# Performance work log

Hardware: AMD Instinct MI355X
Metric: run time of the kernel (lower is better)

The kernel has to match this reference:

```python
import jax, jax.numpy as jnp
import numpy as np

RADIUS = 2  # half window; original kernel truncates the spatial Gaussian at ~2.5*sigma


def setup_inputs() -> dict:
    key = jax.random.key(0)
    input_img = jax.random.normal(key, (2, 1, 128, 128, 128), dtype=jnp.float32)
    return {
        "input_img": input_img,
        "sigma_x": jnp.float32(1.0),
        "sigma_y": jnp.float32(1.0),
        "sigma_z": jnp.float32(1.0),
        "color_sigma": jnp.float32(0.5),
    }


def reference(input_img, sigma_x, sigma_y, sigma_z, color_sigma):
    # 3D bilateral filter: out(i) = sum_k w_spatial(k) * w_range(x_i, x_k) * x_k / sum_k w
    R = RADIUS
    pad = [(0, 0), (0, 0), (R, R), (R, R), (R, R)]
    xp = jnp.pad(input_img, pad)                       # zero-padded volume
    mp = jnp.pad(jnp.ones_like(input_img), pad)        # validity mask (out-of-bounds taps excluded)

    offs = np.array([(dx, dy, dz)
                     for dx in range(-R, R + 1)
                     for dy in range(-R, R + 1)
                     for dz in range(-R, R + 1)], dtype=np.int32)  # (K,3), K=125
    d2 = jnp.asarray(offs.astype(np.float32) ** 2)     # squared offsets (K,3)
    w_sp = jnp.exp(-(d2[:, 0] / (2.0 * sigma_x ** 2)
                     + d2[:, 1] / (2.0 * sigma_y ** 2)
                     + d2[:, 2] / (2.0 * sigma_z ** 2)))  # (K,)
    starts = jnp.asarray(offs + R)                     # slice starts into the padded volume

    inv_2cs2 = 1.0 / (2.0 * color_sigma ** 2)
    shape = input_img.shape

    def body(carry, inp):
        num, den = carry
        start, ws = inp
        s = jnp.concatenate([jnp.zeros(2, jnp.int32), start])
        xk = jax.lax.dynamic_slice(xp, s, shape)       # shifted neighbor volume
        mk = jax.lax.dynamic_slice(mp, s, shape)
        w = ws * mk * jnp.exp(-(input_img - xk) ** 2 * inv_2cs2)
        return (num + w * xk, den + w), None

    zero = jnp.zeros_like(input_img)
    (num, den), _ = jax.lax.scan(body, (zero, zero), (starts, w_sp))
    return num / den
```

## Files before the change

### kernel.cpp

```cpp
#include <hip/hip_runtime.h>
#include <hip/hip_bf16.h>


#define RADIUS 2
#define N 128
#define TX 16
#define TY 8
#define TZ 8
#define PITCH (TX + 2 * RADIUS)
#define LYD (TY + 2 * RADIUS)
#define LZD (TZ + 2 * RADIUS)
#define LDS_SIZE (PITCH * LYD * LZD)

#define LOG2E 1.4426950408889634f
#define BIG 1.0e18f
#define EXP2_SCALE 8388608.0f
#define EXP2_BIAS 1065353216.0f

typedef float f32x2 __attribute__((ext_vector_type(2)));

__global__ __launch_bounds__(256, 4) void bilateral3d_kernel(
    const float* __restrict__ in, const float* __restrict__ p_sx,
    const float* __restrict__ p_sy, const float* __restrict__ p_sz,
    const float* __restrict__ p_cs, float* __restrict__ out) {
  __shared__ float s[LDS_SIZE];

  const int tid = threadIdx.x;
  const int x0 = blockIdx.x * TX;
  const int y0 = blockIdx.y * TY;
  const int zb = blockIdx.z;
  const int z0 = (zb & 15) * TZ;
  const int b = zb >> 4;

  const float* vol = in + (size_t)b * (N * N * N);

  for (int i = tid; i < LDS_SIZE; i += 256) {
    int lx = i % PITCH;
    int t = i / PITCH;
    int ly = t % LYD;
    int lz = t / LYD;
    int gx = x0 + lx - RADIUS;
    int gy = y0 + ly - RADIUS;
    int gz = z0 + lz - RADIUS;
    float v = BIG;
    if ((unsigned)gx < N && (unsigned)gy < N && (unsigned)gz < N)
      v = vol[((size_t)gz * N + gy) * N + gx];
    s[i] = v;
  }
  __syncthreads();

  const int tx = tid & 3;
  const int ty = (tid >> 2) & 7;
  const int tz = tid >> 5;

  const float sxv = p_sx[0], syv = p_sy[0], szv = p_sz[0], csv = p_cs[0];
  const float AX2 = EXP2_SCALE * LOG2E / (2.0f * sxv * sxv);
  const float AY2 = EXP2_SCALE * LOG2E / (2.0f * syv * syv);
  const float AZ2 = EXP2_SCALE * LOG2E / (2.0f * szv * szv);
  const float AX2_4 = 4.0f * AX2;
  const float sR = __builtin_sqrtf(EXP2_SCALE * LOG2E / (2.0f * csv * csv));
  f32x2 S2;
  S2.x = sR;
  S2.y = sR;

  const int xw = 4 * tx;

  const int cbase = ((tz + RADIUS) * LYD + (ty + RADIUS)) * PITCH + xw;
  const float xs0 = s[cbase + 2] * sR;
  const float xs1 = s[cbase + 3] * sR;
  const float xs2 = s[cbase + 4] * sR;
  const float xs3 = s[cbase + 5] * sR;
  f32x2 XS0, XS1, XS2, XS3;
  XS0.x = xs0; XS0.y = xs0;
  XS1.x = xs1; XS1.y = xs1;
  XS2.x = xs2; XS2.y = xs2;
  XS3.x = xs3; XS3.y = xs3;

  f32x2 NU0 = {0.f, 0.f}, NU1 = {0.f, 0.f}, NU2 = {0.f, 0.f}, NU3 = {0.f, 0.f};
  f32x2 DE0 = {0.f, 0.f}, DE1 = {0.f, 0.f}, DE2 = {0.f, 0.f}, DE3 = {0.f, 0.f};
  float ns0 = 0, ns1 = 0, ns2 = 0, ns3 = 0;
  float es0 = 0, es1 = 0, es2 = 0, es3 = 0;

#define PK(XS2V, GS, GR, CC2, NUM2, DEN2)                                \
  {                                                                      \
    f32x2 _t, _e;                                                        \
    asm("v_pk_add_f32 %0, %1, %2 neg_lo:[0,1] neg_hi:[0,1]"              \
        : "=v"(_t) : "v"(XS2V), "v"(GS));                                \
    asm("v_pk_fma_f32 %0, %1, %1, %2 neg_lo:[0,1,0] neg_hi:[0,1,0]"      \
        : "=v"(_e) : "v"(_t), "v"(CC2));                                 \
    unsigned _ql, _qh;                                                   \
    asm("v_cvt_u32_f32 %0, %1" : "=v"(_ql) : "v"(_e.x));                 \
    asm("v_cvt_u32_f32 %0, %1" : "=v"(_qh) : "v"(_e.y));                 \
    f32x2 _w;                                                            \
    _w.x = __uint_as_float(_ql);                                         \
    _w.y = __uint_as_float(_qh);                                         \
    asm("v_pk_add_f32 %0, %0, %1" : "+v"(DEN2) : "v"(_w));               \
    asm("v_pk_fma_f32 %0, %1, %2, %0" : "+v"(NUM2) : "v"(_w), "v"(GR));  \
  }

#define SC(XSV, FS, FR, CC, NN, EE)                      \
  {                                                      \
    float _t = (XSV) - (FS);                             \
    float _f = fmaf(_t, -_t, (CC));                      \
    unsigned _q;                                         \
    asm("v_cvt_u32_f32 %0, %1" : "=v"(_q) : "v"(_f));    \
    float _w = __uint_as_float(_q);                      \
    EE += _w;                                            \
    NN = fmaf(_w, (FR), NN);                             \
  }

#pragma unroll 1
  for (int dz = -RADIUS; dz <= RADIUS; ++dz) {
    const float pz2 = AZ2 * (float)(dz * dz);
    const int zrow = (tz + RADIUS + dz) * LYD;
#pragma unroll
    for (int dy = -RADIUS; dy <= RADIUS; ++dy) {
      const float cc0 = EXP2_BIAS - (pz2 + AY2 * (float)(dy * dy));
      const float cm1 = cc0 - AX2;
      const float cm4 = cc0 - AX2_4;
      f32x2 P41, P01, P10, P14;
      P41.x = cm4; P41.y = cm1;
      P01.x = cc0; P01.y = cm1;
      P10.x = cm1; P10.y = cc0;
      P14.x = cm1; P14.y = cm4;

      const int rb = (zrow + (ty + RADIUS + dy)) * PITCH + xw;
      const f32x2 G0 = *(const f32x2*)&s[rb];
      const f32x2 G1 = *(const f32x2*)&s[rb + 2];
      const f32x2 G2 = *(const f32x2*)&s[rb + 4];
      const f32x2 G3 = *(const f32x2*)&s[rb + 6];
      f32x2 Gs0, Gs1, Gs2, Gs3;
      asm("v_pk_mul_f32 %0, %1, %2" : "=v"(Gs0) : "v"(G0), "v"(S2));
      asm("v_pk_mul_f32 %0, %1, %2" : "=v"(Gs1) : "v"(G1), "v"(S2));
      asm("v_pk_mul_f32 %0, %1, %2" : "=v"(Gs2) : "v"(G2), "v"(S2));
      asm("v_pk_mul_f32 %0, %1, %2" : "=v"(Gs3) : "v"(G3), "v"(S2));

      PK(XS0, Gs0, G0, P41, NU0, DE0)
      PK(XS0, Gs1, G1, P01, NU0, DE0)
      SC(xs0, Gs2.x, G2.x, cm4, ns0, es0)
      SC(xs1, Gs0.y, G0.y, cm4, ns1, es1)
      PK(XS1, Gs1, G1, P10, NU1, DE1)
      PK(XS1, Gs2, G2, P14, NU1, DE1)
      PK(XS2, Gs1, G1, P41, NU2, DE2)
      PK(XS2, Gs2, G2, P01, NU2, DE2)
      SC(xs2, Gs3.x, G3.x, cm4, ns2, es2)
      SC(xs3, Gs1.y, G1.y, cm4, ns3, es3)
      PK(XS3, Gs2, G2, P10, NU3, DE3)
      PK(XS3, Gs3, G3, P14, NU3, DE3)
    }
  }

  float4 r;
  r.x = (NU0.x + NU0.y + ns0) / (DE0.x + DE0.y + es0);
  r.y = (NU1.x + NU1.y + ns1) / (DE1.x + DE1.y + es1);
  r.z = (NU2.x + NU2.y + ns2) / (DE2.x + DE2.y + es2);
  r.w = (NU3.x + NU3.y + ns3) / (DE3.x + DE3.y + es3);

  const int gz = z0 + tz, gy = y0 + ty;
  *(float4*)&out[(((size_t)b * N + gz) * N + gy) * N + (x0 + xw)] = r;
}

extern "C" void kernel_launch(void* const* d_in, const int* in_sizes, int n_in,
                              void* d_out, int out_size, void* d_ws, size_t ws_size,
                              hipStream_t stream) {
  const float* in = (const float*)d_in[0];
  const float* sx = (const float*)d_in[1];
  const float* sy = (const float*)d_in[2];
  const float* sz = (const float*)d_in[3];
  const float* cs = (const float*)d_in[4];
  float* out = (float*)d_out;

  dim3 grid(N / TX, N / TY, (N / TZ) * 2);
  bilateral3d_kernel<<<grid, 256, 0, stream>>>(in, sx, sy, sz, cs, out);
}
```

Measured before the change: 137.6 us.

## Use fp16 exponent-trick weights and packed fp16 accumulation in bilateral filter

Pre-scales the LDS tile by the range sigma when loading and stores an extra fp16 copy of it. The exp2 trick now builds fp16 bit patterns: a fmax against a magic constant plus a byte perm packs two weights into one register, replacing the float-to-uint converts. Numerator and denominator are accumulated with packed fp16 add and fma, which cuts VALU work per tap. In exchange, fp16 accumulation over 125 taps loses precision and the weight approximation gets coarser, which may exceed the accuracy tolerance.

```diff
diff --git a/kernel.cpp b/kernel.cpp
--- a/kernel.cpp
+++ b/kernel.cpp
@@ -14,16 +14,27 @@
 
 #define LOG2E 1.4426950408889634f
 #define BIG 1.0e18f
-#define EXP2_SCALE 8388608.0f
-#define EXP2_BIAS 1065353216.0f
+#define MAGIC 8388608.0f
+#define BASE16 8403968.0f
 
 typedef float f32x2 __attribute__((ext_vector_type(2)));
+typedef _Float16 h16x2 __attribute__((ext_vector_type(2)));
+
+static __device__ __forceinline__ float lo_f(unsigned u) {
+  h16x2 t = __builtin_bit_cast(h16x2, u);
+  return (float)t.x;
+}
+static __device__ __forceinline__ float hi_f(unsigned u) {
+  h16x2 t = __builtin_bit_cast(h16x2, u);
+  return (float)t.y;
+}
 
 __global__ __launch_bounds__(256, 4) void bilateral3d_kernel(
     const float* __restrict__ in, const float* __restrict__ p_sx,
     const float* __restrict__ p_sy, const float* __restrict__ p_sz,
     const float* __restrict__ p_cs, float* __restrict__ out) {
   __shared__ float s[LDS_SIZE];
+  __shared__ _Float16 h[LDS_SIZE];
 
   const int tid = threadIdx.x;
   const int x0 = blockIdx.x * TX;
@@ -31,6 +42,14 @@
   const int zb = blockIdx.z;
   const int z0 = (zb & 15) * TZ;
   const int b = zb >> 4;
+
+  const float sxv = p_sx[0], syv = p_sy[0], szv = p_sz[0], csv = p_cs[0];
+  const float K10 = 1024.0f * LOG2E;
+  const float AX2 = K10 / (2.0f * sxv * sxv);
+  const float AY2 = K10 / (2.0f * syv * syv);
+  const float AZ2 = K10 / (2.0f * szv * szv);
+  const float AX2_4 = 4.0f * AX2;
+  const float sR = __builtin_sqrtf(K10 / (2.0f * csv * csv));
 
   const float* vol = in + (size_t)b * (N * N * N);
 
@@ -45,7 +64,9 @@
     float v = BIG;
     if ((unsigned)gx < N && (unsigned)gy < N && (unsigned)gz < N)
       v = vol[((size_t)gz * N + gy) * N + gx];
-    s[i] = v;
+    float vs = v * sR;
+    s[i] = vs;
+    h[i] = (_Float16)__builtin_fminf(vs, 60000.0f);
   }
   __syncthreads();
 
@@ -53,60 +74,50 @@
   const int ty = (tid >> 2) & 7;
   const int tz = tid >> 5;
 
-  const float sxv = p_sx[0], syv = p_sy[0], szv = p_sz[0], csv = p_cs[0];
-  const float AX2 = EXP2_SCALE * LOG2E / (2.0f * sxv * sxv);
-  const float AY2 = EXP2_SCALE * LOG2E / (2.0f * syv * syv);
-  const float AZ2 = EXP2_SCALE * LOG2E / (2.0f * szv * szv);
-  const float AX2_4 = 4.0f * AX2;
-  const float sR = __builtin_sqrtf(EXP2_SCALE * LOG2E / (2.0f * csv * csv));
-  f32x2 S2;
-  S2.x = sR;
-  S2.y = sR;
-
   const int xw = 4 * tx;
 
   const int cbase = ((tz + RADIUS) * LYD + (ty + RADIUS)) * PITCH + xw;
-  const float xs0 = s[cbase + 2] * sR;
-  const float xs1 = s[cbase + 3] * sR;
-  const float xs2 = s[cbase + 4] * sR;
-  const float xs3 = s[cbase + 5] * sR;
+  const float xs0 = s[cbase + 2];
+  const float xs1 = s[cbase + 3];
+  const float xs2 = s[cbase + 4];
+  const float xs3 = s[cbase + 5];
   f32x2 XS0, XS1, XS2, XS3;
   XS0.x = xs0; XS0.y = xs0;
   XS1.x = xs1; XS1.y = xs1;
   XS2.x = xs2; XS2.y = xs2;
   XS3.x = xs3; XS3.y = xs3;
 
-  f32x2 NU0 = {0.f, 0.f}, NU1 = {0.f, 0.f}, NU2 = {0.f, 0.f}, NU3 = {0.f, 0.f};
-  f32x2 DE0 = {0.f, 0.f}, DE1 = {0.f, 0.f}, DE2 = {0.f, 0.f}, DE3 = {0.f, 0.f};
-  float ns0 = 0, ns1 = 0, ns2 = 0, ns3 = 0;
-  float es0 = 0, es1 = 0, es2 = 0, es3 = 0;
-
-#define PK(XS2V, GS, GR, CC2, NUM2, DEN2)                                \
-  {                                                                      \
-    f32x2 _t, _e;                                                        \
-    asm("v_pk_add_f32 %0, %1, %2 neg_lo:[0,1] neg_hi:[0,1]"              \
-        : "=v"(_t) : "v"(XS2V), "v"(GS));                                \
-    asm("v_pk_fma_f32 %0, %1, %1, %2 neg_lo:[0,1,0] neg_hi:[0,1,0]"      \
-        : "=v"(_e) : "v"(_t), "v"(CC2));                                 \
-    unsigned _ql, _qh;                                                   \
-    asm("v_cvt_u32_f32 %0, %1" : "=v"(_ql) : "v"(_e.x));                 \
-    asm("v_cvt_u32_f32 %0, %1" : "=v"(_qh) : "v"(_e.y));                 \
-    f32x2 _w;                                                            \
-    _w.x = __uint_as_float(_ql);                                         \
-    _w.y = __uint_as_float(_qh);                                         \
-    asm("v_pk_add_f32 %0, %0, %1" : "+v"(DEN2) : "v"(_w));               \
-    asm("v_pk_fma_f32 %0, %1, %2, %0" : "+v"(NUM2) : "v"(_w), "v"(GR));  \
-  }
-
-#define SC(XSV, FS, FR, CC, NN, EE)                      \
-  {                                                      \
-    float _t = (XSV) - (FS);                             \
-    float _f = fmaf(_t, -_t, (CC));                      \
-    unsigned _q;                                         \
-    asm("v_cvt_u32_f32 %0, %1" : "=v"(_q) : "v"(_f));    \
-    float _w = __uint_as_float(_q);                      \
-    EE += _w;                                            \
-    NN = fmaf(_w, (FR), NN);                             \
+  const unsigned* hw = (const unsigned*)h;
+
+  unsigned NUa0 = 0, NUa1 = 0, NUa2 = 0, NUa3 = 0;
+  unsigned DEa0 = 0, DEa1 = 0, DEa2 = 0, DEa3 = 0;
+  unsigned NUs01 = 0, NUs23 = 0, DEs01 = 0, DEs23 = 0;
+
+#define PK(XS2V, GS, H16, CC2, NUM, DEN)                                   \
+  {                                                                        \
+    f32x2 _t, _y;                                                          \
+    asm("v_pk_add_f32 %0, %1, %2 neg_lo:[0,1] neg_hi:[0,1]"                \
+        : "=v"(_t) : "v"(XS2V), "v"(GS));                                  \
+    asm("v_pk_fma_f32 %0, %1, %1, %2 neg_lo:[0,1,0] neg_hi:[0,1,0]"        \
+        : "=v"(_y) : "v"(_t), "v"(CC2));                                   \
+    float _ax = __builtin_fmaxf(_y.x, MAGIC);                              \
+    float _ay = __builtin_fmaxf(_y.y, MAGIC);                              \
+    unsigned _w = __builtin_amdgcn_perm(__float_as_uint(_ay),              \
+                                        __float_as_uint(_ax), 0x05040100); \
+    asm("v_pk_add_f16 %0, %0, %1" : "+v"(DEN) : "v"(_w));                  \
+    asm("v_pk_fma_f16 %0, %1, %2, %0" : "+v"(NUM) : "v"(_w), "v"(H16));    \
+  }
+
+#define SC2(XA, XB, GA, GB, H16, CC, NUM, DEN)                             \
+  {                                                                        \
+    float _ta = (XA) - (GA);                                               \
+    float _tb = (XB) - (GB);                                               \
+    float _ya = __builtin_fmaxf(fmaf(_ta, -_ta, (CC)), MAGIC);             \
+    float _yb = __builtin_fmaxf(fmaf(_tb, -_tb, (CC)), MAGIC);             \
+    unsigned _w = __builtin_amdgcn_perm(__float_as_uint(_yb),              \
+                                        __float_as_uint(_ya), 0x05040100); \
+    asm("v_pk_add_f16 %0, %0, %1" : "+v"(DEN) : "v"(_w));                  \
+    asm("v_pk_fma_f16 %0, %1, %2, %0" : "+v"(NUM) : "v"(_w), "v"(H16));    \
   }
 
 #pragma unroll 1
@@ -115,7 +126,7 @@
     const int zrow = (tz + RADIUS + dz) * LYD;
 #pragma unroll
     for (int dy = -RADIUS; dy <= RADIUS; ++dy) {
-      const float cc0 = EXP2_BIAS - (pz2 + AY2 * (float)(dy * dy));
+      const float cc0 = BASE16 - (pz2 + AY2 * (float)(dy * dy));
       const float cm1 = cc0 - AX2;
       const float cm4 = cc0 - AX2_4;
       f32x2 P41, P01, P10, P14;
@@ -129,32 +140,46 @@
       const f32x2 G1 = *(const f32x2*)&s[rb + 2];
       const f32x2 G2 = *(const f32x2*)&s[rb + 4];
       const f32x2 G3 = *(const f32x2*)&s[rb + 6];
-      f32x2 Gs0, Gs1, Gs2, Gs3;
-      asm("v_pk_mul_f32 %0, %1, %2" : "=v"(Gs0) : "v"(G0), "v"(S2));
-      asm("v_pk_mul_f32 %0, %1, %2" : "=v"(Gs1) : "v"(G1), "v"(S2));
-      asm("v_pk_mul_f32 %0, %1, %2" : "=v"(Gs2) : "v"(G2), "v"(S2));
-      asm("v_pk_mul_f32 %0, %1, %2" : "=v"(Gs3) : "v"(G3), "v"(S2));
-
-      PK(XS0, Gs0, G0, P41, NU0, DE0)
-      PK(XS0, Gs1, G1, P01, NU0, DE0)
-      SC(xs0, Gs2.x, G2.x, cm4, ns0, es0)
-      SC(xs1, Gs0.y, G0.y, cm4, ns1, es1)
-      PK(XS1, Gs1, G1, P10, NU1, DE1)
-      PK(XS1, Gs2, G2, P14, NU1, DE1)
-      PK(XS2, Gs1, G1, P41, NU2, DE2)
-      PK(XS2, Gs2, G2, P01, NU2, DE2)
-      SC(xs2, Gs3.x, G3.x, cm4, ns2, es2)
-      SC(xs3, Gs1.y, G1.y, cm4, ns3, es3)
-      PK(XS3, Gs2, G2, P10, NU3, DE3)
-      PK(XS3, Gs3, G3, P14, NU3, DE3)
+      const int hb = rb >> 1;
+      const unsigned H0 = hw[hb];
+      const unsigned H1 = hw[hb + 1];
+      const unsigned H2 = hw[hb + 2];
+      const unsigned H3 = hw[hb + 3];
+
+      PK(XS0, G0, H0, P41, NUa0, DEa0)
+      PK(XS0, G1, H1, P01, NUa0, DEa0)
+      PK(XS1, G1, H1, P10, NUa1, DEa1)
+      PK(XS1, G2, H2, P14, NUa1, DEa1)
+      PK(XS2, G1, H1, P41, NUa2, DEa2)
+      PK(XS2, G2, H2, P01, NUa2, DEa2)
+      PK(XS3, G2, H2, P10, NUa3, DEa3)
+      PK(XS3, G3, H3, P14, NUa3, DEa3)
+
+      {
+        unsigned Ga16 = __builtin_amdgcn_perm(H0, H2, 0x07060100);
+        SC2(xs0, xs1, G2.x, G0.y, Ga16, cm4, NUs01, DEs01)
+      }
+      {
+        unsigned Gb16 = __builtin_amdgcn_perm(H1, H3, 0x07060100);
+        SC2(xs2, xs3, G3.x, G1.y, Gb16, cm4, NUs23, DEs23)
+      }
     }
   }
 
+  const float num0 = lo_f(NUa0) + hi_f(NUa0) + lo_f(NUs01);
+  const float num1 = lo_f(NUa1) + hi_f(NUa1) + hi_f(NUs01);
+  const float num2 = lo_f(NUa2) + hi_f(NUa2) + lo_f(NUs23);
+  const float num3 = lo_f(NUa3) + hi_f(NUa3) + hi_f(NUs23);
+  const float den0 = lo_f(DEa0) + hi_f(DEa0) + lo_f(DEs01);
+  const float den1 = lo_f(DEa1) + hi_f(DEa1) + hi_f(DEs01);
+  const float den2 = lo_f(DEa2) + hi_f(DEa2) + lo_f(DEs23);
+  const float den3 = lo_f(DEa3) + hi_f(DEa3) + hi_f(DEs23);
+
   float4 r;
-  r.x = (NU0.x + NU0.y + ns0) / (DE0.x + DE0.y + es0);
-  r.y = (NU1.x + NU1.y + ns1) / (DE1.x + DE1.y + es1);
-  r.z = (NU2.x + NU2.y + ns2) / (DE2.x + DE2.y + es2);
-  r.w = (NU3.x + NU3.y + ns3) / (DE3.x + DE3.y + es3);
+  r.x = num0 / (den0 * sR);
+  r.y = num1 / (den1 * sR);
+  r.z = num2 / (den2 * sR);
+  r.w = num3 / (den3 * sR);
 
   const int gz = z0 + tz, gy = y0 + ty;
   *(float4*)&out[(((size_t)b * N + gz) * N + gy) * N + (x0 + xw)] = r;
```

Measured after the change: 149.7 us. 1.09x slower.
